# Kernel tuning notes

Hardware: AMD Instinct MI355X
Metric: run time of the kernel (lower is better)

The kernel has to match this reference:

```python
import jax, jax.numpy as jnp
import numpy as np

EPS = 1e-08


def setup_inputs() -> dict:
    key = jax.random.key(0)
    k1, k2 = jax.random.split(key)
    B, N = 64, 1024
    lower = jax.random.normal(k1, (B, N), dtype=jnp.float32)
    # upper >= lower; gap ~ U[0,2) so we get active (l>=0), inactive (u<=0), and crossing neurons
    upper = lower + 2.0 * jax.random.uniform(k2, (B, N), dtype=jnp.float32)
    return {"lower": lower, "upper": upper}


def reference(lower, upper):
    # Concrete interval bounds through ReLU
    concrete_lower = jnp.maximum(lower, 0.0)
    concrete_upper = jnp.maximum(upper, 0.0)

    active = lower >= 0                      # [B, N] identity relaxation
    crossing = (lower < 0) & (upper > 0)     # [B, N] linear upper relaxation

    lambda_upper = jnp.where(crossing, upper / (upper - lower + EPS), 0.0)  # [B, N]
    mu_upper = jnp.where(crossing, -lambda_upper * lower, 0.0)              # [B, N]

    # Per-neuron diagonal coefficients (only the diagonal is ever nonzero)
    lower_diag = active.astype(lower.dtype)                       # 1 if active else 0
    upper_diag = jnp.where(active, jnp.ones_like(lambda_upper), lambda_upper)

    n = lower.shape[1]
    eye = jnp.eye(n, dtype=lower.dtype)                           # [N, N]
    lower_coef = eye * lower_diag[:, :, None]                     # [B, N, N] dense diagonal
    upper_coef = eye * upper_diag[:, :, None]                     # [B, N, N] dense diagonal

    lower_bias = jnp.zeros_like(lower)
    upper_bias = mu_upper

    return (concrete_lower, concrete_upper, lower_coef, upper_coef, lower_bias, upper_bias)
```

## Files before the change

### kernel.cpp

```cpp
#include <hip/hip_runtime.h>

#define EPS 1e-8f


__global__ void diag_small_kernel(const float* __restrict__ lower,
                                  const float* __restrict__ upper,
                                  float* __restrict__ out) {
    const int BN = 65536;
    int t = blockIdx.x * blockDim.x + threadIdx.x;
    if (t >= 2 * BN) return;
    int rr = t & (BN - 1);
    int i  = rr & 1023;
    float l = lower[rr];
    float u = upper[rr];
    bool active   = (l >= 0.0f);
    bool crossing = (l < 0.0f) && (u > 0.0f);
    float lam = crossing ? u / (u - l + EPS) : 0.0f;

    float v = active ? 1.0f : (t < BN ? 0.0f : lam);
    if (v != 0.0f) {
        out[131072LL + (long long)t * 1024 + i] = v;
    }

    if (t < BN) {
        float mu = crossing ? -lam * l : 0.0f;
        out[t]                  = fmaxf(l, 0.0f);
        out[BN + t]             = fmaxf(u, 0.0f);
        out[134414336LL + t]    = mu;
    }
}

extern "C" void kernel_launch(void* const* d_in, const int* in_sizes, int n_in,
                              void* d_out, int out_size, void* d_ws, size_t ws_size,
                              hipStream_t stream) {
    const float* lower = (const float*)d_in[0];
    const float* upper = (const float*)d_in[1];
    float* out = (float*)d_out;

    hipMemsetAsync(out + 131072, 0, 134283264ULL * sizeof(float), stream);

    diag_small_kernel<<<512, 256, 0, stream>>>(lower, upper, out);
}
```

Measured before the change: 101.9 us.

## Fuse zero-fill and diagonal writes into one row-per-wave vectorized kernel

Replaces the separate memset plus scattered diagonal store kernel with one kernel where each wavefront writes entire 1024-float rows using 16-byte vector stores, inserting the diagonal value in-register. Small outputs (concrete bounds, zero bias, mu) are handled as extra virtual rows with vectorized loads. This removes one launch and the second pass of partial-line writes over the diagonal, at the cost of relying on the kernel's store throughput instead of the driver memset.

```diff
diff --git a/kernel.cpp b/kernel.cpp
--- a/kernel.cpp
+++ b/kernel.cpp
@@ -2,31 +2,93 @@
 
 #define EPS 1e-8f
 
+typedef float f32x4 __attribute__((ext_vector_type(4)));
 
-__global__ void diag_small_kernel(const float* __restrict__ lower,
-                                  const float* __restrict__ upper,
-                                  float* __restrict__ out) {
-    const int BN = 65536;
-    int t = blockIdx.x * blockDim.x + threadIdx.x;
-    if (t >= 2 * BN) return;
-    int rr = t & (BN - 1);
-    int i  = rr & 1023;
-    float l = lower[rr];
-    float u = upper[rr];
-    bool active   = (l >= 0.0f);
-    bool crossing = (l < 0.0f) && (u > 0.0f);
-    float lam = crossing ? u / (u - l + EPS) : 0.0f;
 
-    float v = active ? 1.0f : (t < BN ? 0.0f : lam);
-    if (v != 0.0f) {
-        out[131072LL + (long long)t * 1024 + i] = v;
-    }
+__global__ void __launch_bounds__(256)
+fused_kernel(const float* __restrict__ lower,
+             const float* __restrict__ upper,
+             float* __restrict__ out) {
+    const int lane = threadIdx.x & 63;
+    const int W = blockIdx.x * 4 + (threadIdx.x >> 6);
+    const int start = W * 16 + (W < 256 ? W : 256);
+    const int count = (W < 256) ? 17 : 16;
 
-    if (t < BN) {
-        float mu = crossing ? -lam * l : 0.0f;
-        out[t]                  = fmaxf(l, 0.0f);
-        out[BN + t]             = fmaxf(u, 0.0f);
-        out[134414336LL + t]    = mu;
+    for (int ri = 0; ri < count; ++ri) {
+        const int vr = start + ri;
+        if (vr < 131072) {
+            const int rr = vr & 65535;
+            const float l = lower[rr];
+            const float u = upper[rr];
+            const bool active = (l >= 0.0f);
+            const bool crossing = (l < 0.0f) && (u > 0.0f);
+            const float lam = crossing ? u / (u - l + EPS) : 0.0f;
+            const float v = active ? 1.0f : (vr < 65536 ? 0.0f : lam);
+            const int i = vr & 1023;
+            f32x4* rp = (f32x4*)(out + 131072 + (size_t)vr * 1024) + lane;
+            const int base = lane * 4;
+#pragma unroll
+            for (int k = 0; k < 4; ++k) {
+                const int b = base + k * 256;
+                f32x4 z;
+                z.x = (b + 0 == i) ? v : 0.0f;
+                z.y = (b + 1 == i) ? v : 0.0f;
+                z.z = (b + 2 == i) ? v : 0.0f;
+                z.w = (b + 3 == i) ? v : 0.0f;
+                rp[k * 64] = z;
+            }
+        } else if (vr < 131136) {
+            f32x4* rp = (f32x4*)(out + 134348800LL +
+                                 (size_t)(vr - 131072) * 1024) + lane;
+            const f32x4 z = {0.0f, 0.0f, 0.0f, 0.0f};
+#pragma unroll
+            for (int k = 0; k < 4; ++k) rp[k * 64] = z;
+        } else if (vr < 131200) {
+            const int r = vr - 131136;
+            const f32x4* lp = (const f32x4*)(lower + (size_t)r * 1024) + lane;
+            f32x4* rp = (f32x4*)(out + (size_t)r * 1024) + lane;
+#pragma unroll
+            for (int k = 0; k < 4; ++k) {
+                f32x4 a = lp[k * 64];
+                a.x = fmaxf(a.x, 0.0f);
+                a.y = fmaxf(a.y, 0.0f);
+                a.z = fmaxf(a.z, 0.0f);
+                a.w = fmaxf(a.w, 0.0f);
+                rp[k * 64] = a;
+            }
+        } else if (vr < 131264) {
+            const int r = vr - 131200;
+            const f32x4* up = (const f32x4*)(upper + (size_t)r * 1024) + lane;
+            f32x4* rp = (f32x4*)(out + 65536 + (size_t)r * 1024) + lane;
+#pragma unroll
+            for (int k = 0; k < 4; ++k) {
+                f32x4 a = up[k * 64];
+                a.x = fmaxf(a.x, 0.0f);
+                a.y = fmaxf(a.y, 0.0f);
+                a.z = fmaxf(a.z, 0.0f);
+                a.w = fmaxf(a.w, 0.0f);
+                rp[k * 64] = a;
+            }
+        } else {
+            const int r = vr - 131264;
+            const f32x4* lp = (const f32x4*)(lower + (size_t)r * 1024) + lane;
+            const f32x4* up = (const f32x4*)(upper + (size_t)r * 1024) + lane;
+            f32x4* rp = (f32x4*)(out + 134414336LL + (size_t)r * 1024) + lane;
+#pragma unroll
+            for (int k = 0; k < 4; ++k) {
+                f32x4 lv = lp[k * 64];
+                f32x4 uv = up[k * 64];
+                f32x4 m;
+#pragma unroll
+                for (int e = 0; e < 4; ++e) {
+                    float l = lv[e], u = uv[e];
+                    bool crossing = (l < 0.0f) && (u > 0.0f);
+                    float lam = crossing ? u / (u - l + EPS) : 0.0f;
+                    m[e] = crossing ? -lam * l : 0.0f;
+                }
+                rp[k * 64] = m;
+            }
+        }
     }
 }
 
@@ -37,7 +99,5 @@
     const float* upper = (const float*)d_in[1];
     float* out = (float*)d_out;
 
-    hipMemsetAsync(out + 131072, 0, 134283264ULL * sizeof(float), stream);
-
-    diag_small_kernel<<<512, 256, 0, stream>>>(lower, upper, out);
+    fused_kernel<<<2048, 256, 0, stream>>>(lower, upper, out);
 }
```

After: 122.3 us. 20.1% more time.
